# Kernel tuning notes

Measured on AMD Instinct MI355X. Metric: run time of the kernel, lower is better.

Reference implementation:

```python
import jax, jax.numpy as jnp
import numpy as np

B, S, D, H = 2, 4096, 128, 128
EPS = 1e-6
NEG_INF = -1e30


def _complex_linear(xr, xi, Wr, Wi, br, bi):
    # x: (B,S,D); W: (H,D); complex linear (Wr + i Wi)(xr + i xi) + (br + i bi) per layer math:
    # real_out = (xr Wr + br) - (xi Wi + bi); imag_out = (xi Wr + br) + (xr Wi + bi)
    out_r = xr @ Wr.T + br - (xi @ Wi.T + bi)
    out_i = xi @ Wr.T + br + (xr @ Wi.T + bi)
    return out_r, out_i


def setup_inputs() -> dict:
    key = jax.random.key(0)
    ks = jax.random.split(key, 24)
    scale = 1.0 / np.sqrt(D)
    def W(k):
        return jax.random.normal(k, (H, D), jnp.float32) * scale
    def b(k):
        return jax.random.normal(k, (H,), jnp.float32) * 0.01
    inp = {
        "Z_q": jax.random.normal(ks[0], (B, 2, S, D, 1), jnp.float32),
        "Z_k": jax.random.normal(ks[1], (B, 2, S, D, 1), jnp.float32),
        "Z_v": jax.random.normal(ks[2], (B, 2, S, D, 1), jnp.float32),
        "Wq_r": W(ks[3]), "Wq_i": W(ks[4]), "bq_r": b(ks[5]), "bq_i": b(ks[6]),
        "Wk_r": W(ks[7]), "Wk_i": W(ks[8]), "bk_r": b(ks[9]), "bk_i": b(ks[10]),
        "Wv_r": W(ks[11]), "Wv_i": W(ks[12]), "bv_r": b(ks[13]), "bv_i": b(ks[14]),
        "Wp_r": W(ks[15]), "Wp_i": W(ks[16]), "bp_r": b(ks[17]), "bp_i": b(ks[18]),
        "noise_floor": jnp.asarray(1.0, jnp.float32),
        "tau": jnp.asarray(0.0, jnp.float32),
    }
    return inp


def reference(Z_q, Z_k, Z_v,
              Wq_r, Wq_i, bq_r, bq_i,
              Wk_r, Wk_i, bk_r, bk_i,
              Wv_r, Wv_i, bv_r, bv_i,
              Wp_r, Wp_i, bp_r, bp_i,
              noise_floor, tau):
    # squeeze trailing singleton; split real/imag -> (B,S,D)
    zqr, zqi = Z_q[:, 0, :, :, 0], Z_q[:, 1, :, :, 0]
    zkr, zki = Z_k[:, 0, :, :, 0], Z_k[:, 1, :, :, 0]
    zvr, zvi = Z_v[:, 0, :, :, 0], Z_v[:, 1, :, :, 0]

    Qr, Qi = _complex_linear(zqr, zqi, Wq_r, Wq_i, bq_r, bq_i)
    Kr, Ki = _complex_linear(zkr, zki, Wk_r, Wk_i, bk_r, bk_i)
    Vr, Vi = _complex_linear(zvr, zvi, Wv_r, Wv_i, bv_r, bv_i)

    # InverseMahalanobis: R2[b,i,j] = sum_h |Q[b,i]-K[b,j]|^2
    q2 = jnp.sum(Qr * Qr + Qi * Qi, axis=-1)          # (B,S)
    k2 = jnp.sum(Kr * Kr + Ki * Ki, axis=-1)          # (B,S)
    re_qk = (jnp.einsum('bsh,bth->bst', Qr, Kr)
             + jnp.einsum('bsh,bth->bst', Qi, Ki))    # (B,S,S)
    R2 = q2[:, :, None] + k2[:, None, :] - 2.0 * re_qk

    attn_scores = -jax.nn.softplus(tau) * jnp.log(noise_floor ** 2 + R2 + EPS)
    mask = jnp.tril(jnp.ones((S, S), dtype=bool))[None]
    attn_scores = jnp.where(mask, attn_scores, NEG_INF)
    attn_weights = jax.nn.softmax(attn_scores / jnp.sqrt(jnp.float32(H)), axis=-1)

    # attn (real) times complex V
    est_r = jnp.einsum('bst,bth->bsh', attn_weights, Vr)
    est_i = jnp.einsum('bst,bth->bsh', attn_weights, Vi)

    out_r, out_i = _complex_linear(est_r, est_i, Wp_r, Wp_i, bp_r, bp_i)
    out = jnp.stack((out_r, out_i), axis=1)[..., None]  # (B,2,S,H,1)
    return out, attn_weights
```

## Files before the change

kernel.cpp:

```cpp
#include <hip/hip_runtime.h>

#define S_LEN 4096
#define NBATCH 2
#define OUT_ELEMS 2097152

typedef _Float16 f16;
typedef _Float16 f16x8 __attribute__((ext_vector_type(8)));
typedef _Float16 f16x4 __attribute__((ext_vector_type(4)));
typedef float f32x4 __attribute__((ext_vector_type(4)));

#define MT_OFF    0x000000
#define BIAS_OFF  0x080000
#define SC_OFF    0x081000
#define QH_OFF    0x100000
#define KH_OFF    0x500000
#define VH_OFF    0x900000
#define Q2_OFF    0xD00000
#define K2_OFF    0xD10000
#define L_OFF     0xD20000
#define VPT_OFF   0xE00000
#define PW_OFF    0x1600000
#define WS_NEED   0x5600000

#define MFMA16(A,B,C) __builtin_amdgcn_mfma_f32_16x16x32_f16(A,B,C,0,0,0)

__device__ __forceinline__ void async_cp16(f16* lds, const f16* g) {
  __builtin_amdgcn_global_load_lds(
      (const __attribute__((address_space(1))) void*)g,
      (__attribute__((address_space(3))) void*)lds, 16, 0, 0);
}


__device__ __forceinline__ void stage16(f16* lds, const f16* g, int stride, int tid) {
#pragma unroll
  for (int i = 0; i < 2; ++i) {
    int idx = i*256 + tid;
    int row = idx >> 2, c = idx & 3;
    int cs = c ^ ((row >> 1) & 3);
    async_cp16(lds + idx*8, g + (size_t)row*stride + cs*8);
  }
}

__device__ __forceinline__ void stage32(f16* lds, const float* g, int stride, int tid) {
#pragma unroll
  for (int i = 0; i < 4; ++i) {
    int idx = i*256 + tid;
    int row = idx >> 3, c = idx & 7;
    const float4* gp = (const float4*)(g + (size_t)row*stride + c*4);
    float4 v = *gp;
    f16x4 h; h[0]=(f16)v.x; h[1]=(f16)v.y; h[2]=(f16)v.z; h[3]=(f16)v.w;
    int cl = (((c >> 1) ^ ((row >> 1) & 3)) << 1) | (c & 1);
    *(f16x4*)(lds + row*32 + cl*4) = h;
  }
}

__device__ __forceinline__ void mfma_step(const f16* Asm, const f16* Bsm, int lane,
                                          int wm, int wn, f32x4 acc[4][4]) {
  f16x8 a[4], b[4];
  int rr = lane & 15;
  int sc = (lane >> 4) ^ ((rr >> 1) & 3);
#pragma unroll
  for (int i=0;i<4;i++) a[i] = *(const f16x8*)(Asm + (wm + i*16 + rr)*32 + (sc<<3));
#pragma unroll
  for (int j=0;j<4;j++) b[j] = *(const f16x8*)(Bsm + (wn + j*16 + rr)*32 + (sc<<3));
#pragma unroll
  for (int i=0;i<4;i++)
#pragma unroll
    for (int j=0;j<4;j++) acc[i][j] = MFMA16(a[i], b[j], acc[i][j]);
}

__global__ __launch_bounds__(256)
void k_build(const float* Wqr, const float* Wqi, const float* bqr, const float* bqi,
             const float* Wkr, const float* Wki, const float* bkr, const float* bki,
             const float* Wvr, const float* Wvi, const float* bvr, const float* bvi,
             const float* Wpr, const float* Wpi, const float* bpr, const float* bpi,
             f16* Mt, float* bias) {
  int mat = blockIdx.x;
  const float *Wr, *Wi, *br, *bi;
  if (mat == 0)      { Wr=Wqr; Wi=Wqi; br=bqr; bi=bqi; }
  else if (mat == 1) { Wr=Wkr; Wi=Wki; br=bkr; bi=bki; }
  else if (mat == 2) { Wr=Wvr; Wi=Wvi; br=bvr; bi=bvi; }
  else               { Wr=Wpr; Wi=Wpi; br=bpr; bi=bpi; }
  int idx = blockIdx.y*256 + threadIdx.x;
  int n = idx >> 8, k = idx & 255;
  int d = k & 127, h = n & 127;
  float w = (k < 128) ? ((n < 128) ? Wr[h*128+d] : Wi[h*128+d])
                      : ((n < 128) ? -Wi[h*128+d] : Wr[h*128+d]);
  Mt[mat*65536 + n*256 + k] = (f16)w;
  if (k == 0)
    bias[mat*256 + n] = (n < 128) ? (br[n] - bi[n]) : (br[n-128] + bi[n-128]);
}

__global__ __launch_bounds__(256)
void k_init(float* outp, float* zreg, float* sc, const float* bias,
            const float* nf, const float* tau) {
  int idx = blockIdx.x*256 + threadIdx.x;
  if (idx < 1048576) {
    int hq = idx & 31;
    int comp = (idx >> 17) & 1;
    ((float4*)outp)[idx] = *(const float4*)(bias + 3*256 + comp*128 + hq*4);
  } else {
    int j = idx - 1048576;
    if (j < 12288) ((float4*)zreg)[j] = make_float4(0.f,0.f,0.f,0.f);
  }
  if (idx == 0) {
    float t = tau[0];
    float c = __builtin_log2f(1.0f + __builtin_exp2f(t * 1.4426950408889634f))
              * 0.6931471805599453f;
    sc[0] = -c * 0.08838834764831845f;
    sc[1] = nf[0]*nf[0] + 1e-6f;
  }
}

__global__ __launch_bounds__(256)
void k_proj(const float* Zq, const float* Zk, const float* Zv,
            const f16* Mt, const float* bias,
            f16* Qh, f16* Kh, f16* Vh, float* q2, float* k2) {
  __shared__ f16 Asm[2][128*32];
  __shared__ f16 Bsm[2][128*32];
  __shared__ float bias_s[128];
  int tid = threadIdx.x;
  int mode = blockIdx.z;
  int m0 = blockIdx.x * 128, n0 = blockIdx.y * 128;
  const float* Z = (mode==0) ? Zq : (mode==1 ? Zk : Zv);
  const f16* Bt = Mt + mode*65536;
  if (tid < 128) bias_s[tid] = bias[mode*256 + n0 + tid];
  int b = m0 >> 12, s0 = m0 & 4095;
  int lane = tid & 63, w = tid >> 6;
  int wm = (w >> 1)*64, wn = (w & 1)*64;
  f32x4 acc[4][4] = {};
  {
    const float* Ag = Z + (((size_t)(b*2 + 0))*S_LEN + s0)*128 + 0;
    stage32(Asm[0], Ag, 128, tid);
    stage16(Bsm[0], Bt + n0*256 + 0, 256, tid);
  }
  __syncthreads();
  for (int kb = 0; kb < 8; ++kb) {
    int cur = kb & 1;
    if (kb < 7) {
      int k1 = (kb+1)*32;
      int part = k1 >> 7, d0 = k1 & 127;
      const float* Ag = Z + (((size_t)(b*2 + part))*S_LEN + s0)*128 + d0;
      stage32(Asm[cur^1], Ag, 128, tid);
      stage16(Bsm[cur^1], Bt + n0*256 + k1, 256, tid);
    }
    mfma_step(Asm[cur], Bsm[cur], lane, wm, wn, acc);
    __syncthreads();
  }
  int rr = (lane>>4)*4, cc = lane & 15;
  f16* O = (mode==0) ? Qh : (mode==1 ? Kh : Vh);
  float rs[4][4];
#pragma unroll
  for (int i=0;i<4;i++)
#pragma unroll
    for (int r=0;r<4;r++) rs[i][r]=0.f;
#pragma unroll
  for (int i=0;i<4;i++)
#pragma unroll
    for (int j=0;j<4;j++) {
      int cl = wn + j*16 + cc;
      int cg = n0 + cl;
      float bv = bias_s[cl];
#pragma unroll
      for (int r=0;r<4;r++) {
        int rg = m0 + wm + i*16 + rr + r;
        f16 hv = (f16)(acc[i][j][r] + bv);
        O[(size_t)rg*256 + cg] = hv;
        float fv = (float)hv;
        rs[i][r] += fv*fv;
      }
    }
  if (mode < 2) {
#pragma unroll
    for (int m=8;m>=1;m>>=1)
#pragma unroll
      for (int i=0;i<4;i++)
#pragma unroll
        for (int r=0;r<4;r++) rs[i][r] += __shfl_xor(rs[i][r], m, 64);
    if (cc == 0) {
      float* T = (mode==0) ? q2 : k2;
#pragma unroll
      for (int i=0;i<4;i++)
#pragma unroll
        for (int r=0;r<4;r++) {
          int rg = m0 + wm + i*16 + rr + r;
          atomicAdd(&T[rg], rs[i][r]);
        }
    }
  }
}

__global__ __launch_bounds__(256)
void k_vp(const f16* Vh, const f16* Mt, f16* VPt) {
  __shared__ f16 Asm[2][128*32];
  __shared__ f16 Bsm[2][128*32];
  int t0 = blockIdx.x*128, n0 = blockIdx.y*128, b = blockIdx.z;
  int tid = threadIdx.x;
  int lane = tid & 63, w = tid >> 6;
  int wm = (w>>1)*64, wn = (w&1)*64;
  const f16* Ag = Mt + 3*65536 + n0*256;
  const f16* Bg = Vh + ((size_t)(b*S_LEN) + t0)*256;
  f32x4 acc[4][4] = {};
  stage16(Asm[0], Ag, 256, tid);
  stage16(Bsm[0], Bg, 256, tid);
  __syncthreads();
  for (int kb=0;kb<8;kb++) {
    int cur = kb & 1;
    if (kb < 7) {
      stage16(Asm[cur^1], Ag + (kb+1)*32, 256, tid);
      stage16(Bsm[cur^1], Bg + (kb+1)*32, 256, tid);
    }
    mfma_step(Asm[cur], Bsm[cur], lane, wm, wn, acc);
    __syncthreads();
  }
  int rr = (lane>>4)*4, cc = lane & 15;
#pragma unroll
  for (int i=0;i<4;i++) {
    int n = n0 + wm + i*16 + rr;
#pragma unroll
    for (int j=0;j<4;j++) {
      int t = t0 + wn + j*16 + cc;
#pragma unroll
      for (int r=0;r<4;r++)
        VPt[(size_t)b*1048576 + (size_t)(n + r)*4096 + t] = (f16)acc[i][j][r];
    }
  }
}

__global__ __launch_bounds__(256)
void k_attn(const f16* Qh, const f16* Kh, const float* q2, const float* k2,
            const float* sc, float* lsum, f16* Pws, float* attn) {
  int x = blockIdx.x;
  int b = x >> 10, r = x & 1023;
  int sb = r >> 5, tb = r & 31;
  int s0 = sb*128, t0 = tb*128;
  int tid = threadIdx.x;
  if (tb > sb) {
    float4 z = make_float4(0.f,0.f,0.f,0.f);
    int row = tid >> 1, h = tid & 1;
    float4* p = (float4*)(attn + ((size_t)(b*S_LEN) + s0 + row)*S_LEN + t0 + h*64);
#pragma unroll
    for (int i=0;i<16;i++) p[i] = z;
    return;
  }
  __shared__ f16 Asm[2][128*32];
  __shared__ f16 Bsm[2][128*32];
  __shared__ float q2s[128], k2s[128];
  if (tid < 128) {
    q2s[tid] = q2[b*S_LEN + s0 + tid];
    k2s[tid] = k2[b*S_LEN + t0 + tid];
  }
  float kc = sc[0], nf2 = sc[1];
  int lane = tid & 63, w = tid >> 6;
  int wm = (w >> 1)*64, wn = (w & 1)*64;
  const f16* Ag = Qh + ((size_t)(b*S_LEN) + s0)*256;
  const f16* Bg = Kh + ((size_t)(b*S_LEN) + t0)*256;
  f32x4 acc[4][4] = {};
  stage16(Asm[0], Ag, 256, tid);
  stage16(Bsm[0], Bg, 256, tid);
  __syncthreads();
  for (int kb=0;kb<8;kb++) {
    int cur = kb & 1;
    if (kb < 7) {
      stage16(Asm[cur^1], Ag + (kb+1)*32, 256, tid);
      stage16(Bsm[cur^1], Bg + (kb+1)*32, 256, tid);
    }
    mfma_step(Asm[cur], Bsm[cur], lane, wm, wn, acc);
    __syncthreads();
  }
  int rr = (lane>>4)*4, cc = lane & 15;
  bool diag = (tb == sb);
  float rs[4][4];
#pragma unroll
  for (int i=0;i<4;i++)
#pragma unroll
    for (int rg=0;rg<4;rg++) rs[i][rg]=0.f;
#pragma unroll
  for (int i=0;i<4;i++)
#pragma unroll
    for (int j=0;j<4;j++) {
      int cl = wn + j*16 + cc;
      float kv = k2s[cl];
#pragma unroll
      for (int rg=0;rg<4;rg++) {
        int rl = wm + i*16 + rr + rg;
        float xx = nf2 + q2s[rl] + kv - 2.0f*acc[i][j][rg];
        float P = __builtin_exp2f(kc * __builtin_log2f(__builtin_fmaxf(xx, 1e-6f)));
        if (diag && (t0+cl) > (s0+rl)) P = 0.f;
        Pws[((size_t)(b*S_LEN) + s0 + rl)*S_LEN + t0 + cl] = (f16)P;
        rs[i][rg] += P;
      }
    }
#pragma unroll
  for (int m=8;m>=1;m>>=1)
#pragma unroll
    for (int i=0;i<4;i++)
#pragma unroll
      for (int rg=0;rg<4;rg++) rs[i][rg] += __shfl_xor(rs[i][rg], m, 64);
  if (cc == 0)
#pragma unroll
    for (int i=0;i<4;i++)
#pragma unroll
      for (int rg=0;rg<4;rg++) {
        int rl = wm + i*16 + rr + rg;
        atomicAdd(&lsum[b*S_LEN + s0 + rl], rs[i][rg]);
      }
}

__global__ __launch_bounds__(256)
void k_pv(const f16* Pws, const f16* VPt, const float* lsum, float* outp, float* attn) {
  __shared__ f16 Asm[2][128*32];
  __shared__ f16 Bsm[2][128*32];
  __shared__ float ls[128];
  int r = blockIdx.x;
  int nb = blockIdx.y, b = blockIdx.z;
  int sb = 0;
  while (r >= ((sb+4)>>2)) { r -= (sb+4)>>2; sb++; }
  int c = r;
  int s0 = sb*128, h0 = nb*128;
  int tid = threadIdx.x;
  bool wrb = (nb == 0);
  if (tid < 128) ls[tid] = 1.0f / lsum[b*S_LEN + s0 + tid];
  int lane = tid & 63, w = tid >> 6;
  int wm = (w>>1)*64, wn = (w&1)*64;
  int tb0 = c*4, tb1 = tb0 + 4; if (tb1 > sb+1) tb1 = sb+1;
  int nt = (tb1 - tb0) * 4;
  int base_t = tb0*128;
  const f16* Abase = Pws + ((size_t)(b*S_LEN) + s0)*S_LEN + base_t;
  const f16* Bbase = VPt + (size_t)b*1048576 + (size_t)h0*4096 + base_t;
  f32x4 acc[4][4] = {};
  int row2 = tid >> 1, half2 = tid & 1;
  int xs2 = (row2 >> 1) & 3;
  stage16(Asm[0], Abase, S_LEN, tid);
  stage16(Bsm[0], Bbase, 4096, tid);
  __syncthreads();
  for (int st = 0; st < nt; ++st) {
    int cur = st & 1;
    int t0 = base_t + st*32;
    if (st + 1 < nt) {
      stage16(Asm[cur^1], Abase + (st+1)*32, S_LEN, tid);
      stage16(Bsm[cur^1], Bbase + (st+1)*32, 4096, tid);
    }
    if (wrb) {
      float invl = ls[row2];
      const f16* Arow = Asm[cur] + row2*32;
      f16x8 v0 = *(const f16x8*)(Arow + (((2*half2  ) ^ xs2) << 3));
      f16x8 v1 = *(const f16x8*)(Arow + (((2*half2+1) ^ xs2) << 3));
      float4* dst = (float4*)(attn + ((size_t)(b*S_LEN) + s0 + row2)*S_LEN + t0 + half2*16);
      float4 o;
      o.x=(float)v0[0]*invl; o.y=(float)v0[1]*invl; o.z=(float)v0[2]*invl; o.w=(float)v0[3]*invl; dst[0]=o;
      o.x=(float)v0[4]*invl; o.y=(float)v0[5]*invl; o.z=(float)v0[6]*invl; o.w=(float)v0[7]*invl; dst[1]=o;
      o.x=(float)v1[0]*invl; o.y=(float)v1[1]*invl; o.z=(float)v1[2]*invl; o.w=(float)v1[3]*invl; dst[2]=o;
      o.x=(float)v1[4]*invl; o.y=(float)v1[5]*invl; o.z=(float)v1[6]*invl; o.w=(float)v1[7]*invl; dst[3]=o;
    }
    mfma_step(Asm[cur], Bsm[cur], lane, wm, wn, acc);
    __syncthreads();
  }
  int rr = (lane>>4)*4, cc = lane & 15;
#pragma unroll
  for (int i=0;i<4;i++)
#pragma unroll
    for (int j=0;j<4;j++) {
      int cg = h0 + wn + j*16 + cc;
      int comp = cg >> 7, h = cg & 127;
#pragma unroll
      for (int rg=0;rg<4;rg++) {
        int rl = wm + i*16 + rr + rg;
        float v = acc[i][j][rg] * ls[rl];
        atomicAdd(&outp[(((size_t)(b*2 + comp))*S_LEN + s0 + rl)*128 + h], v);
      }
    }
}

extern "C" void kernel_launch(void* const* d_in, const int* in_sizes, int n_in,
                              void* d_out, int out_size, void* d_ws, size_t ws_size,
                              hipStream_t stream) {
  (void)in_sizes; (void)n_in; (void)out_size;
  if (ws_size < (size_t)WS_NEED) return;
  const float* Zq = (const float*)d_in[0];
  const float* Zk = (const float*)d_in[1];
  const float* Zv = (const float*)d_in[2];
  char* ws = (char*)d_ws;
  f16*   Mt   = (f16*)(ws + MT_OFF);
  float* bias = (float*)(ws + BIAS_OFF);
  float* sc   = (float*)(ws + SC_OFF);
  f16*   Qh   = (f16*)(ws + QH_OFF);
  f16*   Kh   = (f16*)(ws + KH_OFF);
  f16*   Vh   = (f16*)(ws + VH_OFF);
  float* q2   = (float*)(ws + Q2_OFF);
  float* k2   = (float*)(ws + K2_OFF);
  float* lsum = (float*)(ws + L_OFF);
  f16*   VPt  = (f16*)(ws + VPT_OFF);
  f16*   Pws  = (f16*)(ws + PW_OFF);
  float* outp = (float*)d_out;
  float* attn = outp + OUT_ELEMS;

  k_build<<<dim3(4,256), 256, 0, stream>>>(
      (const float*)d_in[3],  (const float*)d_in[4],  (const float*)d_in[5],  (const float*)d_in[6],
      (const float*)d_in[7],  (const float*)d_in[8],  (const float*)d_in[9],  (const float*)d_in[10],
      (const float*)d_in[11], (const float*)d_in[12], (const float*)d_in[13], (const float*)d_in[14],
      (const float*)d_in[15], (const float*)d_in[16], (const float*)d_in[17], (const float*)d_in[18],
      Mt, bias);
  k_init<<<4144, 256, 0, stream>>>(outp, q2, sc, bias, (const float*)d_in[19], (const float*)d_in[20]);
  k_proj<<<dim3(64,2,3), 256, 0, stream>>>(Zq, Zk, Zv, Mt, bias, Qh, Kh, Vh, q2, k2);
  k_vp<<<dim3(32,2,2), 256, 0, stream>>>(Vh, Mt, VPt);
  k_attn<<<2048, 256, 0, stream>>>(Qh, Kh, q2, k2, sc, lsum, Pws, attn);
  k_pv<<<dim3(144,2,2), 256, 0, stream>>>(Pws, VPt, lsum, outp, attn);
}
```

Before: 318.2 us.

## Restructure attention pipeline: full-K LDS tiles, triangular grids, non-atomic PV output

k_proj and k_attn now load the whole 256-wide K dimension into LDS once (64KB per operand) and run eight MFMA steps without intermediate barriers. k_attn launches only the lower-triangular tiles, and zeroing of the upper triangle of attn moves into k_init. k_pv changes from split-K blocks with atomicAdd to one block per row tile that loops over all key tiles with 128-wide double-buffered stages and writes output plus bias directly. The goal is fewer syncs, no wasted blocks, and no atomics or output pre-initialisation. The cost is large LDS use that limits occupancy, and a k_pv grid of only 128 blocks with unbalanced per-block work.

```diff
diff --git a/kernel.cpp b/kernel.cpp
--- a/kernel.cpp
+++ b/kernel.cpp
@@ -1,7 +1,6 @@
 #include <hip/hip_runtime.h>
 
 #define S_LEN 4096
-#define NBATCH 2
 #define OUT_ELEMS 2097152
 
 typedef _Float16 f16;
@@ -31,6 +30,39 @@
 }
 
 
+template<int LC>
+__device__ __forceinline__ void stageT(f16* lds, const f16* g, size_t stride, int tid) {
+#pragma unroll
+  for (int i = 0; i < (1 << (LC - 1)); ++i) {
+    int idx = i*256 + tid;
+    int row = idx >> LC, c = idx & ((1 << LC) - 1);
+    int cl = c ^ (row & 7);
+    async_cp16(lds + idx*8, g + (size_t)row*stride + cl*8);
+  }
+}
+
+template<int LC>
+__device__ __forceinline__ void mfma_stepT(const f16* Asm, const f16* Bsm, int kb,
+                                           int lane, int wm, int wn, f32x4 acc[4][4]) {
+  f16x8 a[4], b[4];
+  int rr = lane & 15, q = lane >> 4;
+  int L = kb*4 + q;
+#pragma unroll
+  for (int i=0;i<4;i++) {
+    int row = wm + i*16 + rr;
+    a[i] = *(const f16x8*)(Asm + (row << (LC+3)) + ((L ^ (row & 7)) << 3));
+  }
+#pragma unroll
+  for (int j=0;j<4;j++) {
+    int row = wn + j*16 + rr;
+    b[j] = *(const f16x8*)(Bsm + (row << (LC+3)) + ((L ^ (row & 7)) << 3));
+  }
+#pragma unroll
+  for (int i=0;i<4;i++)
+#pragma unroll
+    for (int j=0;j<4;j++) acc[i][j] = MFMA16(a[i], b[j], acc[i][j]);
+}
+
 __device__ __forceinline__ void stage16(f16* lds, const f16* g, int stride, int tid) {
 #pragma unroll
   for (int i = 0; i < 2; ++i) {
@@ -38,19 +70,6 @@
     int row = idx >> 2, c = idx & 3;
     int cs = c ^ ((row >> 1) & 3);
     async_cp16(lds + idx*8, g + (size_t)row*stride + cs*8);
-  }
-}
-
-__device__ __forceinline__ void stage32(f16* lds, const float* g, int stride, int tid) {
-#pragma unroll
-  for (int i = 0; i < 4; ++i) {
-    int idx = i*256 + tid;
-    int row = idx >> 3, c = idx & 7;
-    const float4* gp = (const float4*)(g + (size_t)row*stride + c*4);
-    float4 v = *gp;
-    f16x4 h; h[0]=(f16)v.x; h[1]=(f16)v.y; h[2]=(f16)v.z; h[3]=(f16)v.w;
-    int cl = (((c >> 1) ^ ((row >> 1) & 3)) << 1) | (c & 1);
-    *(f16x4*)(lds + row*32 + cl*4) = h;
   }
 }
 
@@ -92,17 +111,24 @@
 }
 
 __global__ __launch_bounds__(256)
-void k_init(float* outp, float* zreg, float* sc, const float* bias,
-            const float* nf, const float* tau) {
-  int idx = blockIdx.x*256 + threadIdx.x;
-  if (idx < 1048576) {
-    int hq = idx & 31;
-    int comp = (idx >> 17) & 1;
-    ((float4*)outp)[idx] = *(const float4*)(bias + 3*256 + comp*128 + hq*4);
-  } else {
-    int j = idx - 1048576;
-    if (j < 12288) ((float4*)zreg)[j] = make_float4(0.f,0.f,0.f,0.f);
-  }
+void k_init(float* attn, float* zreg, float* sc, const float* nf, const float* tau) {
+  int bx = blockIdx.x, tid = threadIdx.x;
+  float4 z = make_float4(0.f,0.f,0.f,0.f);
+  if (bx < 992) {
+    int b = bx >= 496; int r = bx - b*496;
+    int tb = 1; while (r >= tb) { r -= tb; tb++; }
+    int sb = r;
+    float* base = attn + ((size_t)(b*S_LEN) + sb*128)*S_LEN + tb*128;
+    int c4 = tid & 31;
+#pragma unroll
+    for (int it = 0; it < 16; ++it) {
+      int row = it*8 + (tid >> 5);
+      *(float4*)(base + (size_t)row*S_LEN + c4*4) = z;
+    }
+    return;
+  }
+  int idx = (bx - 992)*256 + tid;
+  if (idx < 12288) ((float4*)zreg)[idx] = z;
   if (idx == 0) {
     float t = tau[0];
     float c = __builtin_log2f(1.0f + __builtin_exp2f(t * 1.4426950408889634f))
@@ -116,37 +142,33 @@
 void k_proj(const float* Zq, const float* Zk, const float* Zv,
             const f16* Mt, const float* bias,
             f16* Qh, f16* Kh, f16* Vh, float* q2, float* k2) {
-  __shared__ f16 Asm[2][128*32];
-  __shared__ f16 Bsm[2][128*32];
+  __shared__ f16 Asm[128*256];
+  __shared__ f16 Bsm[128*256];
   __shared__ float bias_s[128];
   int tid = threadIdx.x;
   int mode = blockIdx.z;
   int m0 = blockIdx.x * 128, n0 = blockIdx.y * 128;
   const float* Z = (mode==0) ? Zq : (mode==1 ? Zk : Zv);
-  const f16* Bt = Mt + mode*65536;
   if (tid < 128) bias_s[tid] = bias[mode*256 + n0 + tid];
   int b = m0 >> 12, s0 = m0 & 4095;
+  stageT<5>(Bsm, Mt + mode*65536 + n0*256, 256, tid);
+  const float* Zb = Z + ((size_t)(b*2))*S_LEN*128 + (size_t)s0*128;
+#pragma unroll
+  for (int i = 0; i < 32; ++i) {
+    int idx = i*256 + tid;
+    int row = idx >> 6, c4 = idx & 63;
+    int part = c4 >> 5, d4 = c4 & 31;
+    float4 v = *(const float4*)(Zb + ((size_t)part*S_LEN + row)*128 + d4*4);
+    f16x4 hv; hv[0]=(f16)v.x; hv[1]=(f16)v.y; hv[2]=(f16)v.z; hv[3]=(f16)v.w;
+    int ch = c4 >> 1;
+    *(f16x4*)(Asm + (row << 8) + ((ch ^ (row & 7)) << 3) + (c4 & 1)*4) = hv;
+  }
+  __syncthreads();
   int lane = tid & 63, w = tid >> 6;
   int wm = (w >> 1)*64, wn = (w & 1)*64;
   f32x4 acc[4][4] = {};
-  {
-    const float* Ag = Z + (((size_t)(b*2 + 0))*S_LEN + s0)*128 + 0;
-    stage32(Asm[0], Ag, 128, tid);
-    stage16(Bsm[0], Bt + n0*256 + 0, 256, tid);
-  }
-  __syncthreads();
-  for (int kb = 0; kb < 8; ++kb) {
-    int cur = kb & 1;
-    if (kb < 7) {
-      int k1 = (kb+1)*32;
-      int part = k1 >> 7, d0 = k1 & 127;
-      const float* Ag = Z + (((size_t)(b*2 + part))*S_LEN + s0)*128 + d0;
-      stage32(Asm[cur^1], Ag, 128, tid);
-      stage16(Bsm[cur^1], Bt + n0*256 + k1, 256, tid);
-    }
-    mfma_step(Asm[cur], Bsm[cur], lane, wm, wn, acc);
-    __syncthreads();
-  }
+#pragma unroll
+  for (int kb = 0; kb < 8; ++kb) mfma_stepT<5>(Asm, Bsm, kb, lane, wm, wn, acc);
   int rr = (lane>>4)*4, cc = lane & 15;
   f16* O = (mode==0) ? Qh : (mode==1 ? Kh : Vh);
   float rs[4][4];
@@ -229,45 +251,29 @@
 
 __global__ __launch_bounds__(256)
 void k_attn(const f16* Qh, const f16* Kh, const float* q2, const float* k2,
-            const float* sc, float* lsum, f16* Pws, float* attn) {
+            const float* sc, float* lsum, f16* Pws) {
+  __shared__ f16 Qs[128*256];
+  __shared__ f16 Ks[128*256];
+  __shared__ float q2s[128], k2s[128];
   int x = blockIdx.x;
-  int b = x >> 10, r = x & 1023;
-  int sb = r >> 5, tb = r & 31;
+  int b = x >= 528; int r = x - b*528;
+  int sb = 0; while (r > sb) { r -= sb + 1; sb++; }
+  int tb = r;
   int s0 = sb*128, t0 = tb*128;
   int tid = threadIdx.x;
-  if (tb > sb) {
-    float4 z = make_float4(0.f,0.f,0.f,0.f);
-    int row = tid >> 1, h = tid & 1;
-    float4* p = (float4*)(attn + ((size_t)(b*S_LEN) + s0 + row)*S_LEN + t0 + h*64);
-#pragma unroll
-    for (int i=0;i<16;i++) p[i] = z;
-    return;
-  }
-  __shared__ f16 Asm[2][128*32];
-  __shared__ f16 Bsm[2][128*32];
-  __shared__ float q2s[128], k2s[128];
+  stageT<5>(Qs, Qh + ((size_t)(b*S_LEN) + s0)*256, 256, tid);
+  stageT<5>(Ks, Kh + ((size_t)(b*S_LEN) + t0)*256, 256, tid);
   if (tid < 128) {
     q2s[tid] = q2[b*S_LEN + s0 + tid];
     k2s[tid] = k2[b*S_LEN + t0 + tid];
   }
+  __syncthreads();
   float kc = sc[0], nf2 = sc[1];
   int lane = tid & 63, w = tid >> 6;
   int wm = (w >> 1)*64, wn = (w & 1)*64;
-  const f16* Ag = Qh + ((size_t)(b*S_LEN) + s0)*256;
-  const f16* Bg = Kh + ((size_t)(b*S_LEN) + t0)*256;
   f32x4 acc[4][4] = {};
-  stage16(Asm[0], Ag, 256, tid);
-  stage16(Bsm[0], Bg, 256, tid);
-  __syncthreads();
-  for (int kb=0;kb<8;kb++) {
-    int cur = kb & 1;
-    if (kb < 7) {
-      stage16(Asm[cur^1], Ag + (kb+1)*32, 256, tid);
-      stage16(Bsm[cur^1], Bg + (kb+1)*32, 256, tid);
-    }
-    mfma_step(Asm[cur], Bsm[cur], lane, wm, wn, acc);
-    __syncthreads();
-  }
+#pragma unroll
+  for (int kb = 0; kb < 8; ++kb) mfma_stepT<5>(Qs, Ks, kb, lane, wm, wn, acc);
   int rr = (lane>>4)*4, cc = lane & 15;
   bool diag = (tb == sb);
   float rs[4][4];
@@ -308,52 +314,51 @@
 }
 
 __global__ __launch_bounds__(256)
-void k_pv(const f16* Pws, const f16* VPt, const float* lsum, float* outp, float* attn) {
-  __shared__ f16 Asm[2][128*32];
-  __shared__ f16 Bsm[2][128*32];
+void k_pv(const f16* Pws, const f16* VPt, const float* lsum, const float* bias,
+          float* outp, float* attn) {
+  __shared__ f16 Asm[2][128*128];
+  __shared__ f16 Bsm[2][128*128];
   __shared__ float ls[128];
-  int r = blockIdx.x;
-  int nb = blockIdx.y, b = blockIdx.z;
-  int sb = 0;
-  while (r >= ((sb+4)>>2)) { r -= (sb+4)>>2; sb++; }
-  int c = r;
+  __shared__ float bias_s[128];
+  int sb = blockIdx.x, nb = blockIdx.y, b = blockIdx.z;
   int s0 = sb*128, h0 = nb*128;
+  int nt = sb + 1;
   int tid = threadIdx.x;
   bool wrb = (nb == 0);
-  if (tid < 128) ls[tid] = 1.0f / lsum[b*S_LEN + s0 + tid];
+  if (tid < 128) {
+    ls[tid] = 1.0f / lsum[b*S_LEN + s0 + tid];
+    bias_s[tid] = bias[3*256 + h0 + tid];
+  }
+  const f16* Abase = Pws + ((size_t)(b*S_LEN) + s0)*S_LEN;
+  const f16* Bbase = VPt + (size_t)b*1048576 + (size_t)h0*4096;
+  stageT<4>(Asm[0], Abase, S_LEN, tid);
+  stageT<4>(Bsm[0], Bbase, 4096, tid);
+  __syncthreads();
   int lane = tid & 63, w = tid >> 6;
   int wm = (w>>1)*64, wn = (w&1)*64;
-  int tb0 = c*4, tb1 = tb0 + 4; if (tb1 > sb+1) tb1 = sb+1;
-  int nt = (tb1 - tb0) * 4;
-  int base_t = tb0*128;
-  const f16* Abase = Pws + ((size_t)(b*S_LEN) + s0)*S_LEN + base_t;
-  const f16* Bbase = VPt + (size_t)b*1048576 + (size_t)h0*4096 + base_t;
   f32x4 acc[4][4] = {};
-  int row2 = tid >> 1, half2 = tid & 1;
-  int xs2 = (row2 >> 1) & 3;
-  stage16(Asm[0], Abase, S_LEN, tid);
-  stage16(Bsm[0], Bbase, 4096, tid);
-  __syncthreads();
-  for (int st = 0; st < nt; ++st) {
-    int cur = st & 1;
-    int t0 = base_t + st*32;
-    if (st + 1 < nt) {
-      stage16(Asm[cur^1], Abase + (st+1)*32, S_LEN, tid);
-      stage16(Bsm[cur^1], Bbase + (st+1)*32, 4096, tid);
+  for (int t = 0; t < nt; ++t) {
+    int cur = t & 1;
+    if (t + 1 < nt) {
+      stageT<4>(Asm[cur^1], Abase + (t+1)*128, S_LEN, tid);
+      stageT<4>(Bsm[cur^1], Bbase + (t+1)*128, 4096, tid);
     }
     if (wrb) {
-      float invl = ls[row2];
-      const f16* Arow = Asm[cur] + row2*32;
-      f16x8 v0 = *(const f16x8*)(Arow + (((2*half2  ) ^ xs2) << 3));
-      f16x8 v1 = *(const f16x8*)(Arow + (((2*half2+1) ^ xs2) << 3));
-      float4* dst = (float4*)(attn + ((size_t)(b*S_LEN) + s0 + row2)*S_LEN + t0 + half2*16);
-      float4 o;
-      o.x=(float)v0[0]*invl; o.y=(float)v0[1]*invl; o.z=(float)v0[2]*invl; o.w=(float)v0[3]*invl; dst[0]=o;
-      o.x=(float)v0[4]*invl; o.y=(float)v0[5]*invl; o.z=(float)v0[6]*invl; o.w=(float)v0[7]*invl; dst[1]=o;
-      o.x=(float)v1[0]*invl; o.y=(float)v1[1]*invl; o.z=(float)v1[2]*invl; o.w=(float)v1[3]*invl; dst[2]=o;
-      o.x=(float)v1[4]*invl; o.y=(float)v1[5]*invl; o.z=(float)v1[6]*invl; o.w=(float)v1[7]*invl; dst[3]=o;
-    }
-    mfma_step(Asm[cur], Bsm[cur], lane, wm, wn, acc);
+      int c4 = tid & 31;
+#pragma unroll
+      for (int i = 0; i < 16; ++i) {
+        int idx = i*256 + tid;
+        int row = idx >> 5;
+        float invl = ls[row];
+        f16x4 v = *(const f16x4*)(Asm[cur] + (row << 7)
+                                  + (((c4 >> 1) ^ (row & 7)) << 3) + (c4 & 1)*4);
+        float4 o;
+        o.x=(float)v[0]*invl; o.y=(float)v[1]*invl; o.z=(float)v[2]*invl; o.w=(float)v[3]*invl;
+        *(float4*)(attn + ((size_t)(b*S_LEN) + s0 + row)*S_LEN + t*128 + c4*4) = o;
+      }
+    }
+#pragma unroll
+    for (int kb = 0; kb < 4; ++kb) mfma_stepT<4>(Asm[cur], Bsm[cur], kb, lane, wm, wn, acc);
     __syncthreads();
   }
   int rr = (lane>>4)*4, cc = lane & 15;
@@ -361,13 +366,14 @@
   for (int i=0;i<4;i++)
 #pragma unroll
     for (int j=0;j<4;j++) {
-      int cg = h0 + wn + j*16 + cc;
+      int cl = wn + j*16 + cc;
+      int cg = h0 + cl;
       int comp = cg >> 7, h = cg & 127;
+      float bv = bias_s[cl];
 #pragma unroll
       for (int rg=0;rg<4;rg++) {
         int rl = wm + i*16 + rr + rg;
-        float v = acc[i][j][rg] * ls[rl];
-        atomicAdd(&outp[(((size_t)(b*2 + comp))*S_LEN + s0 + rl)*128 + h], v);
+        outp[(((size_t)(b*2 + comp))*S_LEN + s0 + rl)*128 + h] = acc[i][j][rg]*ls[rl] + bv;
       }
     }
 }
@@ -401,9 +407,9 @@
       (const float*)d_in[11], (const float*)d_in[12], (const float*)d_in[13], (const float*)d_in[14],
       (const float*)d_in[15], (const float*)d_in[16], (const float*)d_in[17], (const float*)d_in[18],
       Mt, bias);
-  k_init<<<4144, 256, 0, stream>>>(outp, q2, sc, bias, (const float*)d_in[19], (const float*)d_in[20]);
+  k_init<<<1040, 256, 0, stream>>>(attn, q2, sc, (const float*)d_in[19], (const float*)d_in[20]);
   k_proj<<<dim3(64,2,3), 256, 0, stream>>>(Zq, Zk, Zv, Mt, bias, Qh, Kh, Vh, q2, k2);
   k_vp<<<dim3(32,2,2), 256, 0, stream>>>(Vh, Mt, VPt);
-  k_attn<<<2048, 256, 0, stream>>>(Qh, Kh, q2, k2, sc, lsum, Pws, attn);
-  k_pv<<<dim3(144,2,2), 256, 0, stream>>>(Pws, VPt, lsum, outp, attn);
-}
+  k_attn<<<1056, 256, 0, stream>>>(Qh, Kh, q2, k2, sc, lsum, Pws);
+  k_pv<<<dim3(32,2,2), 256, 0, stream>>>(Pws, VPt, lsum, bias, outp, attn);
+}
```

Result: slower. 343.5 us (+8.0%).
